# Performance work log

Measured on AMD Instinct MI355X. Metric: run time of the kernel, lower is better.

Reference implementation:

```python
import jax, jax.numpy as jnp
import numpy as np

N_NODES = 50000
IN_C = 128
OUT_C = 128
N_EDGES = 1600000
NEG_SLOPE = 0.2
EPS = 1e-16  # matches torch_geometric softmax denominator epsilon


def setup_inputs() -> dict:
    key = jax.random.key(0)
    k1, k2, k3, k4, k5 = jax.random.split(key, 5)
    glorot = 1.0 / np.sqrt(IN_C)
    x = jax.random.normal(k1, (N_NODES, IN_C), dtype=jnp.float32)
    W = jax.random.normal(k2, (IN_C, OUT_C), dtype=jnp.float32) * glorot
    a_src = jax.random.normal(k3, (OUT_C,), dtype=jnp.float32) * glorot
    a_dst = jax.random.normal(k4, (OUT_C,), dtype=jnp.float32) * glorot
    bias = jnp.zeros((OUT_C,), dtype=jnp.float32)
    edge_index = jax.random.randint(k5, (2, N_EDGES), 0, N_NODES, dtype=jnp.int32)
    return {"x": x, "W": W, "a_src": a_src, "a_dst": a_dst,
            "bias": bias, "edge_index": edge_index}


def reference(x, W, a_src, a_dst, bias, edge_index):
    N = x.shape[0]
    # add self loops (GATConv default add_self_loops=True)
    loops = jnp.arange(N, dtype=edge_index.dtype)
    src = jnp.concatenate([edge_index[0], loops])  # [E+N]
    dst = jnp.concatenate([edge_index[1], loops])

    h = x @ W                                      # [N, out]
    alpha_s = h @ a_src                            # [N]
    alpha_d = h @ a_dst                            # [N]

    e = alpha_s[src] + alpha_d[dst]                # [E+N]
    e = jnp.where(e > 0, e, NEG_SLOPE * e)         # leaky_relu

    # neighbor-wise (per destination node) stable softmax
    m = jax.ops.segment_max(e, dst, num_segments=N)
    ex = jnp.exp(e - m[dst])
    denom = jax.ops.segment_sum(ex, dst, num_segments=N)
    alpha = ex / (denom[dst] + EPS)

    # weighted aggregation of source features into destination nodes
    msgs = h[src] * alpha[:, None]                 # [E+N, out]
    out = jax.ops.segment_sum(msgs, dst, num_segments=N) + bias
    return jax.nn.relu(out)
```

## Files before the change

### kernel.cpp

```cpp
#include <hip/hip_runtime.h>
#include <hip/hip_fp16.h>

#define C 128
#define NEG_SLOPE 0.2f
#define SM_EPS 1e-16f
#define BKT_SHIFT 8
#define BKT_MASK 255
#define WP 136

typedef unsigned int uint32;
typedef __attribute__((ext_vector_type(8))) short bf16x8;
typedef __attribute__((ext_vector_type(4))) float f32x4;

static __device__ __forceinline__ unsigned short f2bf(float f) {
    uint32 u = __float_as_uint(f);
    uint32 r = 0x7FFFu + ((u >> 16) & 1u);
    return (unsigned short)((u + r) >> 16);
}
static __device__ __forceinline__ uint32 f2bf2(float lo, float hi) {
    return (uint32)f2bf(lo) | ((uint32)f2bf(hi) << 16);
}
static __device__ __forceinline__ uint32 f2h(float f) {
    __half h = __float2half(f);
    return (uint32)*reinterpret_cast<unsigned short*>(&h);
}
static __device__ __forceinline__ float h2f(uint32 b) {
    unsigned short s = (unsigned short)(b & 0xffffu);
    __half h = *reinterpret_cast<__half*>(&s);
    return __half2float(h);
}

__global__ __launch_bounds__(256) void cvtw_kernel(const float* __restrict__ W,
                                                   uint32* __restrict__ Wf) {
    int gid = blockIdx.x * 256 + threadIdx.x;
    int j2   = gid & 3;
    int lane = (gid >> 2) & 63;
    int tile = gid >> 8;
    int t = tile >> 2, kk = tile & 3;
    int n = t * 16 + (lane & 15);
    int k = kk * 32 + (lane >> 4) * 8 + j2 * 2;
    Wf[gid] = f2bf2(W[k * C + n], W[(k + 1) * C + n]);
}

__global__ __launch_bounds__(256) void gemm_hist_kernel(
    const float* __restrict__ x, const uint32* __restrict__ Wf,
    const float* __restrict__ a_src, const float* __restrict__ a_dst,
    unsigned short* __restrict__ hb, float* __restrict__ as_out,
    float* __restrict__ ad_out, int N,
    const int* __restrict__ dst, int* __restrict__ H,
    int E, int total, int chunkE)
{
    __shared__ __align__(16) unsigned short slice[4][16 * WP];
    __shared__ int lhist[256];

    const int tid  = threadIdx.x;
    const int lane = tid & 63;
    const int w    = tid >> 6;
    const int row0 = blockIdx.x * 64;
    const int m16  = lane & 15;
    const int q    = lane >> 4;

    lhist[tid] = 0;

    const int row = row0 + w * 16 + m16;
    const bool rv = (row < N);
    const float* xr_p = x + (size_t)(rv ? row : 0) * C + q * 8;

    float4 xr[8];
    #pragma unroll
    for (int kk = 0; kk < 4; ++kk) {
        xr[kk * 2]     = rv ? *(const float4*)(xr_p + kk * 32)     : make_float4(0, 0, 0, 0);
        xr[kk * 2 + 1] = rv ? *(const float4*)(xr_p + kk * 32 + 4) : make_float4(0, 0, 0, 0);
    }

    f32x4 acc[8];
    const f32x4 zz = {0.f, 0.f, 0.f, 0.f};
    #pragma unroll
    for (int t = 0; t < 8; ++t) acc[t] = zz;

    #pragma unroll
    for (int kk = 0; kk < 4; ++kk) {
        union { bf16x8 v; uint32 u[4]; } au;
        float4 p0 = xr[kk * 2], p1 = xr[kk * 2 + 1];
        au.u[0] = f2bf2(p0.x, p0.y); au.u[1] = f2bf2(p0.z, p0.w);
        au.u[2] = f2bf2(p1.x, p1.y); au.u[3] = f2bf2(p1.z, p1.w);
        #pragma unroll
        for (int t = 0; t < 8; ++t) {
            bf16x8 b = *(const bf16x8*)&Wf[((t * 4 + kk) * 64 + lane) * 4];
            acc[t] = __builtin_amdgcn_mfma_f32_16x16x32_bf16(au.v, b, acc[t], 0, 0, 0);
        }
    }

    float ps[4] = {0.f, 0.f, 0.f, 0.f}, pd[4] = {0.f, 0.f, 0.f, 0.f};
    #pragma unroll
    for (int t = 0; t < 8; ++t) {
        float av = a_src[t * 16 + m16];
        float dv = a_dst[t * 16 + m16];
        #pragma unroll
        for (int r = 0; r < 4; ++r) {
            ps[r] += acc[t][r] * av;
            pd[r] += acc[t][r] * dv;
        }
    }
    #pragma unroll
    for (int r = 0; r < 4; ++r) {
        #pragma unroll
        for (int off = 1; off < 16; off <<= 1) {
            ps[r] += __shfl_xor(ps[r], off, 64);
            pd[r] += __shfl_xor(pd[r], off, 64);
        }
    }
    if (m16 == 0) {
        #pragma unroll
        for (int r = 0; r < 4; ++r) {
            int rr = row0 + w * 16 + q * 4 + r;
            if (rr < N) { as_out[rr] = ps[r]; ad_out[rr] = pd[r]; }
        }
    }

    #pragma unroll
    for (int t = 0; t < 8; ++t)
        #pragma unroll
        for (int r = 0; r < 4; ++r)
            slice[w][(q * 4 + r) * WP + t * 16 + m16] = f2bf(acc[t][r]);
    __syncthreads();
    #pragma unroll
    for (int it = 0; it < 4; ++it) {
        int r = it * 4 + q;
        int rr = row0 + w * 16 + r;
        if (rr < N) {
            bf16x8 v = *(const bf16x8*)&slice[w][r * WP + m16 * 8];
            *(bf16x8*)&hb[(size_t)rr * C + m16 * 8] = v;
        }
    }

    const int c = blockIdx.x;
    const int start = c * chunkE;
    const int end = min(start + chunkE, total);
    for (int i = start + tid; i < end; i += 256) {
        int d = (i < E) ? dst[i] : (i - E);
        atomicAdd(&lhist[d >> BKT_SHIFT], 1);
    }
    __syncthreads();
    H[c * 256 + tid] = lhist[tid];
}

__global__ __launch_bounds__(1024) void scan_cols_kernel(
    int* __restrict__ H, int* __restrict__ colTot, int nchunk)
{
    __shared__ int wt[16];
    const int tid  = threadIdx.x;
    const int lane = tid & 63;
    const int w    = tid >> 6;
    const int col  = blockIdx.x;
    int v = (tid < nchunk) ? H[tid * 256 + col] : 0;
    int x = v;
    #pragma unroll
    for (int o = 1; o < 64; o <<= 1) {
        int t = __shfl_up(x, o, 64);
        if (lane >= o) x += t;
    }
    if (lane == 63) wt[w] = x;
    __syncthreads();
    int wbase = 0;
    #pragma unroll
    for (int w2 = 0; w2 < 16; ++w2) wbase += (w2 < w) ? wt[w2] : 0;
    int e = wbase + x - v;
    if (tid < nchunk) H[tid * 256 + col] = e;
    if (tid == nchunk - 1) colTot[col] = e + v;
}

__global__ __launch_bounds__(256) void scan_off_kernel(
    const int* __restrict__ colTot, int* __restrict__ bucket_off, int total)
{
    __shared__ int wt[4];
    const int tid = threadIdx.x;
    const int lane = tid & 63;
    const int w = tid >> 6;
    int v = colTot[tid];
    int x = v;
    #pragma unroll
    for (int o = 1; o < 64; o <<= 1) {
        int t = __shfl_up(x, o, 64);
        if (lane >= o) x += t;
    }
    if (lane == 63) wt[w] = x;
    __syncthreads();
    int wbase = 0;
    #pragma unroll
    for (int w2 = 0; w2 < 4; ++w2) wbase += (w2 < w) ? wt[w2] : 0;
    bucket_off[tid] = wbase + x - v;
    if (tid == 0) bucket_off[256] = total;
}

__global__ __launch_bounds__(256) void bin_kernel(
    const int* __restrict__ src, const int* __restrict__ dst,
    const int* __restrict__ bucket_off, const int* __restrict__ H,
    uint32* __restrict__ packed, int E, int total, int chunkE)
{
    __shared__ int lhist[256];
    __shared__ int base[256];
    const int tid = threadIdx.x;
    const int c = blockIdx.x;
    const int start = c * chunkE;
    const int end = min(start + chunkE, total);

    lhist[tid] = 0;
    __syncthreads();
    for (int i = start + tid; i < end; i += 256) {
        int d = (i < E) ? dst[i] : (i - E);
        atomicAdd(&lhist[d >> BKT_SHIFT], 1);
    }
    __syncthreads();
    base[tid] = bucket_off[tid] + H[c * 256 + tid];
    lhist[tid] = 0;
    __syncthreads();
    for (int i = start + tid; i < end; i += 256) {
        int s = (i < E) ? src[i] : (i - E);
        int d = (i < E) ? dst[i] : (i - E);
        int b = d >> BKT_SHIFT;
        int pos = base[b] + atomicAdd(&lhist[b], 1);
        packed[pos] = ((uint32)s << BKT_SHIFT) | (uint32)(d & BKT_MASK);
    }
}

__global__ __launch_bounds__(1024) void build_kernel(
    const uint32* __restrict__ packed, const int* __restrict__ bucket_off,
    const float* __restrict__ as, const float* __restrict__ ad,
    int* __restrict__ row_start, uint32* __restrict__ csr, int N, int NB, int total)
{
    __shared__ int cnt[256];
    __shared__ int cur[256];
    __shared__ float adl[256];
    __shared__ int wt[4];
    const int tid = threadIdx.x;
    const int b = blockIdx.x;

    if (tid < 256) {
        cnt[tid] = 0;
        int g = (b << BKT_SHIFT) + tid;
        adl[tid] = (g < N) ? ad[g] : 0.f;
    }
    __syncthreads();
    const int off = bucket_off[b];
    const int end = bucket_off[b + 1];
    if (b == 0 && tid == 0) row_start[N] = total;

    for (int j = off + tid; j < end; j += 1024)
        atomicAdd(&cnt[packed[j] & BKT_MASK], 1);
    __syncthreads();

    int v2 = 0, x2 = 0;
    if (tid < 256) {
        const int lane = tid & 63;
        v2 = cnt[tid]; x2 = v2;
        #pragma unroll
        for (int o = 1; o < 64; o <<= 1) {
            int t = __shfl_up(x2, o, 64);
            if (lane >= o) x2 += t;
        }
        if (lane == 63) wt[tid >> 6] = x2;
    }
    __syncthreads();
    if (tid < 256) {
        const int w = tid >> 6;
        int wbase = 0;
        #pragma unroll
        for (int w2 = 0; w2 < 4; ++w2) wbase += (w2 < w) ? wt[w2] : 0;
        int excl = wbase + x2 - v2;
        int g = (b << BKT_SHIFT) + tid;
        if (g < N) row_start[g] = off + excl;
        cur[tid] = excl;
    }
    __syncthreads();

    for (int j = off + tid; j < end; j += 1024) {
        uint32 p = packed[j];
        int l = (int)(p & BKT_MASK);
        int s = (int)(p >> BKT_SHIFT);
        float e = as[s] + adl[l];
        e = (e > 0.f) ? e : NEG_SLOPE * e;
        int pos = atomicAdd(&cur[l], 1);
        csr[off + pos] = ((uint32)s << 16) | f2h(e);
    }
}

static __device__ __forceinline__ void gather_node_fw(
    int d, const uint32* __restrict__ csr, const int* __restrict__ row_start,
    const unsigned short* __restrict__ hb, const float* __restrict__ bias,
    float* __restrict__ out, int lane)
{
    const int beg = row_start[d];
    const int deg = row_start[d + 1] - beg;
    const int c2 = lane << 1;
    float a0 = 0.f, a1 = 0.f;
    float m = -INFINITY;
    for (int t = lane; t < deg; t += 64) m = fmaxf(m, h2f(csr[beg + t]));
    #pragma unroll
    for (int off = 32; off > 0; off >>= 1) m = fmaxf(m, __shfl_xor(m, off, 64));
    float ssum = 0.f;
    for (int t = lane; t < deg; t += 64) ssum += __expf(h2f(csr[beg + t]) - m);
    #pragma unroll
    for (int off = 32; off > 0; off >>= 1) ssum += __shfl_xor(ssum, off, 64);
    float inv = 1.f / (ssum + SM_EPS);
    for (int t0 = 0; t0 < deg; t0 += 64) {
        int nc = min(64, deg - t0);
        uint32 ent = (lane < nc) ? csr[beg + t0 + lane] : 0xFC00u;
        float wl = (lane < nc) ? __expf(h2f(ent) - m) * inv : 0.f;
        uint32 bc = (ent & 0xffff0000u) | f2h(wl);
        for (int t = 0; t < nc; ++t) {
            uint32 b0 = (uint32)__shfl((int)bc, t, 64);
            uint32 u0 = *(const uint32*)&hb[(size_t)(b0 >> 16) * C + c2];
            float w0 = h2f(b0);
            a0 += __uint_as_float(u0 << 16) * w0;
            a1 += __uint_as_float(u0 & 0xffff0000u) * w0;
        }
    }
    float2 b2 = *(const float2*)&bias[c2];
    a0 = fmaxf(a0 + b2.x, 0.f);
    a1 = fmaxf(a1 + b2.y, 0.f);
    *(float2*)&out[(size_t)d * C + c2] = make_float2(a0, a1);
}

#define ACC4(r, wgt)                                           \
    {                                                          \
        a0 += __uint_as_float((r).x << 16)         * (wgt);    \
        a1 += __uint_as_float((r).x & 0xffff0000u) * (wgt);    \
        a2 += __uint_as_float((r).y << 16)         * (wgt);    \
        a3 += __uint_as_float((r).y & 0xffff0000u) * (wgt);    \
    }

__global__ __launch_bounds__(256) void gather_kernel(
    const uint32* __restrict__ csr, const int* __restrict__ row_start,
    const unsigned short* __restrict__ hb, const float* __restrict__ bias,
    float* __restrict__ out, int N)
{
    __shared__ __align__(16) uint2 lent[4][2][64];
    const int w    = threadIdx.x >> 6;
    const int lane = threadIdx.x & 63;
    const int half = lane >> 5;
    const int hl   = lane & 31;
    const int pair = blockIdx.x * 4 + w;
    const int d0 = pair * 2;
    if (d0 >= N) return;
    const int d = d0 + half;
    const bool valid = (d < N);

    int beg = 0, deg = 0;
    if (valid) { beg = row_start[d]; deg = row_start[d + 1] - beg; }

    int wdeg = deg;
    #pragma unroll
    for (int off = 32; off > 0; off >>= 1) wdeg = max(wdeg, __shfl_xor(wdeg, off, 64));

    if (wdeg > 64) {
        gather_node_fw(d0, csr, row_start, hb, bias, out, lane);
        if (d0 + 1 < N) gather_node_fw(d0 + 1, csr, row_start, hb, bias, out, lane);
        return;
    }

    uint32 ent0 = (hl < deg) ? csr[beg + hl] : 0xFC00u;
    uint32 ent1 = (32 + hl < deg) ? csr[beg + 32 + hl] : 0xFC00u;
    float e0 = h2f(ent0), e1 = h2f(ent1);
    float m = fmaxf(e0, e1);
    #pragma unroll
    for (int off = 16; off > 0; off >>= 1) m = fmaxf(m, __shfl_xor(m, off, 64));
    float p0 = (hl < deg) ? __expf(e0 - m) : 0.f;
    float p1 = (32 + hl < deg) ? __expf(e1 - m) : 0.f;
    float ssum = p0 + p1;
    #pragma unroll
    for (int off = 16; off > 0; off >>= 1) ssum += __shfl_xor(ssum, off, 64);
    const float inv = 1.f / (ssum + SM_EPS);

    lent[w][half][hl]      = make_uint2((ent0 & 0xffff0000u) >> 8, __float_as_uint(p0 * inv));
    lent[w][half][32 + hl] = make_uint2((ent1 & 0xffff0000u) >> 8, __float_as_uint(p1 * inv));
    __builtin_amdgcn_wave_barrier();

    const uint32 cb = (uint32)(hl << 3);
    const char* hbB = (const char*)hb;
    const uint2* lp = &lent[w][half][0];
    float a0 = 0.f, a1 = 0.f, a2 = 0.f, a3 = 0.f;

    int t = 0;
    for (; t + 8 <= deg; t += 8) {
        uint4 q0 = *(const uint4*)(lp + t);
        uint4 q1 = *(const uint4*)(lp + t + 2);
        uint4 q2 = *(const uint4*)(lp + t + 4);
        uint4 q3 = *(const uint4*)(lp + t + 6);
        uint2 r0 = *(const uint2*)(hbB + (q0.x + cb));
        uint2 r1 = *(const uint2*)(hbB + (q0.z + cb));
        uint2 r2 = *(const uint2*)(hbB + (q1.x + cb));
        uint2 r3 = *(const uint2*)(hbB + (q1.z + cb));
        uint2 r4 = *(const uint2*)(hbB + (q2.x + cb));
        uint2 r5 = *(const uint2*)(hbB + (q2.z + cb));
        uint2 r6 = *(const uint2*)(hbB + (q3.x + cb));
        uint2 r7 = *(const uint2*)(hbB + (q3.z + cb));
        float w0 = __uint_as_float(q0.y), w1 = __uint_as_float(q0.w);
        float w2 = __uint_as_float(q1.y), w3 = __uint_as_float(q1.w);
        float w4 = __uint_as_float(q2.y), w5 = __uint_as_float(q2.w);
        float w6 = __uint_as_float(q3.y), w7 = __uint_as_float(q3.w);
        ACC4(r0, w0) ACC4(r1, w1) ACC4(r2, w2) ACC4(r3, w3)
        ACC4(r4, w4) ACC4(r5, w5) ACC4(r6, w6) ACC4(r7, w7)
    }
    for (; t < deg; ++t) {
        uint2 q = lp[t];
        uint2 r = *(const uint2*)(hbB + (q.x + cb));
        float wt = __uint_as_float(q.y);
        ACC4(r, wt)
    }

    if (valid) {
        const int c4 = hl << 2;
        float4 bb = *(const float4*)&bias[c4];
        float4 o;
        o.x = fmaxf(a0 + bb.x, 0.f);
        o.y = fmaxf(a1 + bb.y, 0.f);
        o.z = fmaxf(a2 + bb.z, 0.f);
        o.w = fmaxf(a3 + bb.w, 0.f);
        *(float4*)&out[(size_t)d * C + c4] = o;
    }
}

extern "C" void kernel_launch(void* const* d_in, const int* in_sizes, int n_in,
                              void* d_out, int out_size, void* d_ws, size_t ws_size,
                              hipStream_t stream) {
    const float* x     = (const float*)d_in[0];
    const float* W     = (const float*)d_in[1];
    const float* a_src = (const float*)d_in[2];
    const float* a_dst = (const float*)d_in[3];
    const float* bias  = (const float*)d_in[4];
    const int*   edge  = (const int*)d_in[5];

    const int N = in_sizes[0] / C;
    const int E = in_sizes[5] / 2;
    const int total = E + N;
    const int* src = edge;
    const int* dst = edge + E;
    float* out = (float*)d_out;

    const int NB = (N + BKT_MASK) >> BKT_SHIFT;
    const int ntile = (N + 63) / 64;
    const int chunkE = (total + ntile - 1) / ntile;

    float* ws = (float*)d_ws;
    unsigned short* hb = (unsigned short*)ws;
    float* as = (float*)(hb + (size_t)N * C);
    float* ad = as + N;
    int* row_start = (int*)(ad + N);
    uint32* packed = (uint32*)(row_start + (N + 2));
    uint32* csr    = packed + total;
    uint32* Wf     = csr + total;
    int* colTot    = (int*)(Wf + 8192);
    int* bucket_off = colTot + 256;
    int* H          = bucket_off + 257;

    cvtw_kernel<<<32, 256, 0, stream>>>(W, Wf);
    gemm_hist_kernel<<<ntile, 256, 0, stream>>>(
        x, Wf, a_src, a_dst, hb, as, ad, N, dst, H, E, total, chunkE);
    scan_cols_kernel<<<256, 1024, 0, stream>>>(H, colTot, ntile);
    scan_off_kernel<<<1, 256, 0, stream>>>(colTot, bucket_off, total);
    bin_kernel<<<ntile, 256, 0, stream>>>(
        src, dst, bucket_off, H, packed, E, total, chunkE);
    build_kernel<<<NB, 1024, 0, stream>>>(packed, bucket_off, as, ad, row_start,
                                          csr, N, NB, total);
    gather_kernel<<<((N + 1) / 2 + 3) / 4, 256, 0, stream>>>(csr, row_start, hb, bias, out, N);
}
```

Before: 187.6 us.

## Fold bucket-offset scan into bin/build kernels, drop redundant histogram, widen gather to 4 nodes/wave

Removes the single-block scan_off kernel by having each bin_kernel and build_kernel block recompute the 256-entry bucket offset scan from colTot locally. bin_kernel also drops its first local-histogram pass, which was not needed because the per-chunk offsets already come from H. gather_kernel now handles four destination nodes per wave with 16 lanes each, and each lane loads 16-byte rows covering 8 channels. This aims to cut a kernel launch, one pass over dst, and per-edge load instructions. In exchange the scan work is duplicated in every block, and each node gets fewer lanes for its softmax.

```diff
diff --git a/kernel.cpp b/kernel.cpp
--- a/kernel.cpp
+++ b/kernel.cpp
@@ -170,13 +170,21 @@
     if (tid == nchunk - 1) colTot[col] = e + v;
 }
 
-__global__ __launch_bounds__(256) void scan_off_kernel(
-    const int* __restrict__ colTot, int* __restrict__ bucket_off, int total)
-{
+__global__ __launch_bounds__(256) void bin_kernel(
+    const int* __restrict__ src, const int* __restrict__ dst,
+    const int* __restrict__ colTot, const int* __restrict__ H,
+    uint32* __restrict__ packed, int E, int total, int chunkE)
+{
+    __shared__ int lhist[256];
+    __shared__ int base[256];
     __shared__ int wt[4];
     const int tid = threadIdx.x;
     const int lane = tid & 63;
     const int w = tid >> 6;
+    const int c = blockIdx.x;
+    const int start = c * chunkE;
+    const int end = min(start + chunkE, total);
+
     int v = colTot[tid];
     int x = v;
     #pragma unroll
@@ -185,36 +193,14 @@
         if (lane >= o) x += t;
     }
     if (lane == 63) wt[w] = x;
+    lhist[tid] = 0;
     __syncthreads();
     int wbase = 0;
     #pragma unroll
     for (int w2 = 0; w2 < 4; ++w2) wbase += (w2 < w) ? wt[w2] : 0;
-    bucket_off[tid] = wbase + x - v;
-    if (tid == 0) bucket_off[256] = total;
-}
-
-__global__ __launch_bounds__(256) void bin_kernel(
-    const int* __restrict__ src, const int* __restrict__ dst,
-    const int* __restrict__ bucket_off, const int* __restrict__ H,
-    uint32* __restrict__ packed, int E, int total, int chunkE)
-{
-    __shared__ int lhist[256];
-    __shared__ int base[256];
-    const int tid = threadIdx.x;
-    const int c = blockIdx.x;
-    const int start = c * chunkE;
-    const int end = min(start + chunkE, total);
-
-    lhist[tid] = 0;
-    __syncthreads();
-    for (int i = start + tid; i < end; i += 256) {
-        int d = (i < E) ? dst[i] : (i - E);
-        atomicAdd(&lhist[d >> BKT_SHIFT], 1);
-    }
-    __syncthreads();
-    base[tid] = bucket_off[tid] + H[c * 256 + tid];
-    lhist[tid] = 0;
-    __syncthreads();
+    base[tid] = (wbase + x - v) + H[c * 256 + tid];
+    __syncthreads();
+
     for (int i = start + tid; i < end; i += 256) {
         int s = (i < E) ? src[i] : (i - E);
         int d = (i < E) ? dst[i] : (i - E);
@@ -225,7 +211,7 @@
 }
 
 __global__ __launch_bounds__(1024) void build_kernel(
-    const uint32* __restrict__ packed, const int* __restrict__ bucket_off,
+    const uint32* __restrict__ packed, const int* __restrict__ colTot,
     const float* __restrict__ as, const float* __restrict__ ad,
     int* __restrict__ row_start, uint32* __restrict__ csr, int N, int NB, int total)
 {
@@ -233,17 +219,37 @@
     __shared__ int cur[256];
     __shared__ float adl[256];
     __shared__ int wt[4];
+    __shared__ int boff[257];
     const int tid = threadIdx.x;
     const int b = blockIdx.x;
 
+    int v0 = 0, x0 = 0;
     if (tid < 256) {
+        const int lane = tid & 63;
+        v0 = colTot[tid]; x0 = v0;
+        #pragma unroll
+        for (int o = 1; o < 64; o <<= 1) {
+            int t = __shfl_up(x0, o, 64);
+            if (lane >= o) x0 += t;
+        }
+        if (lane == 63) wt[tid >> 6] = x0;
         cnt[tid] = 0;
         int g = (b << BKT_SHIFT) + tid;
         adl[tid] = (g < N) ? ad[g] : 0.f;
     }
     __syncthreads();
-    const int off = bucket_off[b];
-    const int end = bucket_off[b + 1];
+    if (tid < 256) {
+        const int w = tid >> 6;
+        int wbase = 0;
+        #pragma unroll
+        for (int w2 = 0; w2 < 4; ++w2) wbase += (w2 < w) ? wt[w2] : 0;
+        boff[tid] = wbase + x0 - v0;
+        if (tid == 0) boff[256] = total;
+    }
+    __syncthreads();
+
+    const int off = boff[b];
+    const int end = boff[b + 1];
     if (b == 0 && tid == 0) row_start[N] = total;
 
     for (int j = off + tid; j < end; j += 1024)
@@ -322,12 +328,16 @@
     *(float2*)&out[(size_t)d * C + c2] = make_float2(a0, a1);
 }
 
-#define ACC4(r, wgt)                                           \
+#define ACC8(r, wgt)                                           \
     {                                                          \
         a0 += __uint_as_float((r).x << 16)         * (wgt);    \
         a1 += __uint_as_float((r).x & 0xffff0000u) * (wgt);    \
         a2 += __uint_as_float((r).y << 16)         * (wgt);    \
         a3 += __uint_as_float((r).y & 0xffff0000u) * (wgt);    \
+        a4 += __uint_as_float((r).z << 16)         * (wgt);    \
+        a5 += __uint_as_float((r).z & 0xffff0000u) * (wgt);    \
+        a6 += __uint_as_float((r).w << 16)         * (wgt);    \
+        a7 += __uint_as_float((r).w & 0xffff0000u) * (wgt);    \
     }
 
 __global__ __launch_bounds__(256) void gather_kernel(
@@ -335,15 +345,15 @@
     const unsigned short* __restrict__ hb, const float* __restrict__ bias,
     float* __restrict__ out, int N)
 {
-    __shared__ __align__(16) uint2 lent[4][2][64];
+    __shared__ __align__(16) uint2 lent[4][4][66];
     const int w    = threadIdx.x >> 6;
     const int lane = threadIdx.x & 63;
-    const int half = lane >> 5;
-    const int hl   = lane & 31;
-    const int pair = blockIdx.x * 4 + w;
-    const int d0 = pair * 2;
+    const int qt   = lane >> 4;
+    const int ql   = lane & 15;
+    const int quad = blockIdx.x * 4 + w;
+    const int d0 = quad * 4;
     if (d0 >= N) return;
-    const int d = d0 + half;
+    const int d = d0 + qt;
     const bool valid = (d < N);
 
     int beg = 0, deg = 0;
@@ -354,70 +364,84 @@
     for (int off = 32; off > 0; off >>= 1) wdeg = max(wdeg, __shfl_xor(wdeg, off, 64));
 
     if (wdeg > 64) {
-        gather_node_fw(d0, csr, row_start, hb, bias, out, lane);
-        if (d0 + 1 < N) gather_node_fw(d0 + 1, csr, row_start, hb, bias, out, lane);
+        #pragma unroll
+        for (int k = 0; k < 4; ++k)
+            if (d0 + k < N) gather_node_fw(d0 + k, csr, row_start, hb, bias, out, lane);
         return;
     }
 
-    uint32 ent0 = (hl < deg) ? csr[beg + hl] : 0xFC00u;
-    uint32 ent1 = (32 + hl < deg) ? csr[beg + 32 + hl] : 0xFC00u;
-    float e0 = h2f(ent0), e1 = h2f(ent1);
-    float m = fmaxf(e0, e1);
-    #pragma unroll
-    for (int off = 16; off > 0; off >>= 1) m = fmaxf(m, __shfl_xor(m, off, 64));
-    float p0 = (hl < deg) ? __expf(e0 - m) : 0.f;
-    float p1 = (32 + hl < deg) ? __expf(e1 - m) : 0.f;
-    float ssum = p0 + p1;
-    #pragma unroll
-    for (int off = 16; off > 0; off >>= 1) ssum += __shfl_xor(ssum, off, 64);
+    uint32 ent0 = (ql < deg) ? csr[beg + ql] : 0xFC00u;
+    uint32 ent1 = (16 + ql < deg) ? csr[beg + 16 + ql] : 0xFC00u;
+    uint32 ent2 = (32 + ql < deg) ? csr[beg + 32 + ql] : 0xFC00u;
+    uint32 ent3 = (48 + ql < deg) ? csr[beg + 48 + ql] : 0xFC00u;
+    float e0 = h2f(ent0), e1 = h2f(ent1), e2 = h2f(ent2), e3 = h2f(ent3);
+    float m = fmaxf(fmaxf(e0, e1), fmaxf(e2, e3));
+    #pragma unroll
+    for (int off = 8; off > 0; off >>= 1) m = fmaxf(m, __shfl_xor(m, off, 64));
+    float p0 = (ql < deg) ? __expf(e0 - m) : 0.f;
+    float p1 = (16 + ql < deg) ? __expf(e1 - m) : 0.f;
+    float p2 = (32 + ql < deg) ? __expf(e2 - m) : 0.f;
+    float p3 = (48 + ql < deg) ? __expf(e3 - m) : 0.f;
+    float ssum = (p0 + p1) + (p2 + p3);
+    #pragma unroll
+    for (int off = 8; off > 0; off >>= 1) ssum += __shfl_xor(ssum, off, 64);
     const float inv = 1.f / (ssum + SM_EPS);
 
-    lent[w][half][hl]      = make_uint2((ent0 & 0xffff0000u) >> 8, __float_as_uint(p0 * inv));
-    lent[w][half][32 + hl] = make_uint2((ent1 & 0xffff0000u) >> 8, __float_as_uint(p1 * inv));
+    uint2* lq = &lent[w][qt][0];
+    lq[ql]      = make_uint2((ent0 & 0xffff0000u) >> 8, __float_as_uint(p0 * inv));
+    lq[16 + ql] = make_uint2((ent1 & 0xffff0000u) >> 8, __float_as_uint(p1 * inv));
+    lq[32 + ql] = make_uint2((ent2 & 0xffff0000u) >> 8, __float_as_uint(p2 * inv));
+    lq[48 + ql] = make_uint2((ent3 & 0xffff0000u) >> 8, __float_as_uint(p3 * inv));
     __builtin_amdgcn_wave_barrier();
 
-    const uint32 cb = (uint32)(hl << 3);
+    const uint32 cb = (uint32)(ql << 4);
     const char* hbB = (const char*)hb;
-    const uint2* lp = &lent[w][half][0];
     float a0 = 0.f, a1 = 0.f, a2 = 0.f, a3 = 0.f;
+    float a4 = 0.f, a5 = 0.f, a6 = 0.f, a7 = 0.f;
 
     int t = 0;
     for (; t + 8 <= deg; t += 8) {
-        uint4 q0 = *(const uint4*)(lp + t);
-        uint4 q1 = *(const uint4*)(lp + t + 2);
-        uint4 q2 = *(const uint4*)(lp + t + 4);
-        uint4 q3 = *(const uint4*)(lp + t + 6);
-        uint2 r0 = *(const uint2*)(hbB + (q0.x + cb));
-        uint2 r1 = *(const uint2*)(hbB + (q0.z + cb));
-        uint2 r2 = *(const uint2*)(hbB + (q1.x + cb));
-        uint2 r3 = *(const uint2*)(hbB + (q1.z + cb));
-        uint2 r4 = *(const uint2*)(hbB + (q2.x + cb));
-        uint2 r5 = *(const uint2*)(hbB + (q2.z + cb));
-        uint2 r6 = *(const uint2*)(hbB + (q3.x + cb));
-        uint2 r7 = *(const uint2*)(hbB + (q3.z + cb));
+        uint4 q0 = *(const uint4*)(lq + t);
+        uint4 q1 = *(const uint4*)(lq + t + 2);
+        uint4 q2 = *(const uint4*)(lq + t + 4);
+        uint4 q3 = *(const uint4*)(lq + t + 6);
+        uint4 r0 = *(const uint4*)(hbB + (q0.x + cb));
+        uint4 r1 = *(const uint4*)(hbB + (q0.z + cb));
+        uint4 r2 = *(const uint4*)(hbB + (q1.x + cb));
+        uint4 r3 = *(const uint4*)(hbB + (q1.z + cb));
+        uint4 r4 = *(const uint4*)(hbB + (q2.x + cb));
+        uint4 r5 = *(const uint4*)(hbB + (q2.z + cb));
+        uint4 r6 = *(const uint4*)(hbB + (q3.x + cb));
+        uint4 r7 = *(const uint4*)(hbB + (q3.z + cb));
         float w0 = __uint_as_float(q0.y), w1 = __uint_as_float(q0.w);
         float w2 = __uint_as_float(q1.y), w3 = __uint_as_float(q1.w);
         float w4 = __uint_as_float(q2.y), w5 = __uint_as_float(q2.w);
         float w6 = __uint_as_float(q3.y), w7 = __uint_as_float(q3.w);
-        ACC4(r0, w0) ACC4(r1, w1) ACC4(r2, w2) ACC4(r3, w3)
-        ACC4(r4, w4) ACC4(r5, w5) ACC4(r6, w6) ACC4(r7, w7)
+        ACC8(r0, w0) ACC8(r1, w1) ACC8(r2, w2) ACC8(r3, w3)
+        ACC8(r4, w4) ACC8(r5, w5) ACC8(r6, w6) ACC8(r7, w7)
     }
     for (; t < deg; ++t) {
-        uint2 q = lp[t];
-        uint2 r = *(const uint2*)(hbB + (q.x + cb));
-        float wt = __uint_as_float(q.y);
-        ACC4(r, wt)
+        uint2 qv = lq[t];
+        uint4 r = *(const uint4*)(hbB + (qv.x + cb));
+        float wt2 = __uint_as_float(qv.y);
+        ACC8(r, wt2)
     }
 
     if (valid) {
-        const int c4 = hl << 2;
-        float4 bb = *(const float4*)&bias[c4];
-        float4 o;
-        o.x = fmaxf(a0 + bb.x, 0.f);
-        o.y = fmaxf(a1 + bb.y, 0.f);
-        o.z = fmaxf(a2 + bb.z, 0.f);
-        o.w = fmaxf(a3 + bb.w, 0.f);
-        *(float4*)&out[(size_t)d * C + c4] = o;
+        const int c8 = ql << 3;
+        float4 b0 = *(const float4*)&bias[c8];
+        float4 b1 = *(const float4*)&bias[c8 + 4];
+        float4 o0, o1;
+        o0.x = fmaxf(a0 + b0.x, 0.f);
+        o0.y = fmaxf(a1 + b0.y, 0.f);
+        o0.z = fmaxf(a2 + b0.z, 0.f);
+        o0.w = fmaxf(a3 + b0.w, 0.f);
+        o1.x = fmaxf(a4 + b1.x, 0.f);
+        o1.y = fmaxf(a5 + b1.y, 0.f);
+        o1.z = fmaxf(a6 + b1.z, 0.f);
+        o1.w = fmaxf(a7 + b1.w, 0.f);
+        *(float4*)&out[(size_t)d * C + c8] = o0;
+        *(float4*)&out[(size_t)d * C + c8 + 4] = o1;
     }
 }
 
@@ -451,17 +475,15 @@
     uint32* csr    = packed + total;
     uint32* Wf     = csr + total;
     int* colTot    = (int*)(Wf + 8192);
-    int* bucket_off = colTot + 256;
-    int* H          = bucket_off + 257;
+    int* H         = colTot + 256;
 
     cvtw_kernel<<<32, 256, 0, stream>>>(W, Wf);
     gemm_hist_kernel<<<ntile, 256, 0, stream>>>(
         x, Wf, a_src, a_dst, hb, as, ad, N, dst, H, E, total, chunkE);
     scan_cols_kernel<<<256, 1024, 0, stream>>>(H, colTot, ntile);
-    scan_off_kernel<<<1, 256, 0, stream>>>(colTot, bucket_off, total);
     bin_kernel<<<ntile, 256, 0, stream>>>(
-        src, dst, bucket_off, H, packed, E, total, chunkE);
-    build_kernel<<<NB, 1024, 0, stream>>>(packed, bucket_off, as, ad, row_start,
+        src, dst, colTot, H, packed, E, total, chunkE);
+    build_kernel<<<NB, 1024, 0, stream>>>(packed, colTot, as, ad, row_start,
                                           csr, N, NB, total);
-    gather_kernel<<<((N + 1) / 2 + 3) / 4, 256, 0, stream>>>(csr, row_start, hb, bias, out, N);
-}
+    gather_kernel<<<((N + 3) / 4 + 3) / 4, 256, 0, stream>>>(csr, row_start, hb, bias, out, N);
+}
```

New measurement: 186.9 us. About the same (-0.4%).

## Fuse GEMM with edge binning and fold offset scan into consumers

Applied to the files above, without the earlier changes.

The weight conversion is merged into the histogram kernel, and the feature GEMM is merged with the edge-binning pass. Blocks of the merged kernel are specialized by block index, so the dense GEMM runs alongside the scatter-heavy binning. The separate single-block offset scan kernel is removed: bin blocks and build blocks each recompute the 256-entry prefix scan of bucket totals locally. The redundant per-chunk histogram recount in the binning pass is also dropped. This cuts the launch count and the serialization between stages, at the cost of duplicated small scans in every block.

```diff
diff --git a/kernel.cpp b/kernel.cpp
--- a/kernel.cpp
+++ b/kernel.cpp
@@ -30,111 +30,27 @@
     return __half2float(h);
 }
 
-__global__ __launch_bounds__(256) void cvtw_kernel(const float* __restrict__ W,
-                                                   uint32* __restrict__ Wf) {
-    int gid = blockIdx.x * 256 + threadIdx.x;
-    int j2   = gid & 3;
-    int lane = (gid >> 2) & 63;
-    int tile = gid >> 8;
-    int t = tile >> 2, kk = tile & 3;
-    int n = t * 16 + (lane & 15);
-    int k = kk * 32 + (lane >> 4) * 8 + j2 * 2;
-    Wf[gid] = f2bf2(W[k * C + n], W[(k + 1) * C + n]);
-}
-
-__global__ __launch_bounds__(256) void gemm_hist_kernel(
-    const float* __restrict__ x, const uint32* __restrict__ Wf,
-    const float* __restrict__ a_src, const float* __restrict__ a_dst,
-    unsigned short* __restrict__ hb, float* __restrict__ as_out,
-    float* __restrict__ ad_out, int N,
+__global__ __launch_bounds__(256) void cvtw_hist_kernel(
+    const float* __restrict__ W, uint32* __restrict__ Wf,
     const int* __restrict__ dst, int* __restrict__ H,
-    int E, int total, int chunkE)
-{
-    __shared__ __align__(16) unsigned short slice[4][16 * WP];
+    int E, int total, int nchunk, int chunkE)
+{
     __shared__ int lhist[256];
-
-    const int tid  = threadIdx.x;
-    const int lane = tid & 63;
-    const int w    = tid >> 6;
-    const int row0 = blockIdx.x * 64;
-    const int m16  = lane & 15;
-    const int q    = lane >> 4;
-
+    const int tid = threadIdx.x;
     lhist[tid] = 0;
-
-    const int row = row0 + w * 16 + m16;
-    const bool rv = (row < N);
-    const float* xr_p = x + (size_t)(rv ? row : 0) * C + q * 8;
-
-    float4 xr[8];
-    #pragma unroll
-    for (int kk = 0; kk < 4; ++kk) {
-        xr[kk * 2]     = rv ? *(const float4*)(xr_p + kk * 32)     : make_float4(0, 0, 0, 0);
-        xr[kk * 2 + 1] = rv ? *(const float4*)(xr_p + kk * 32 + 4) : make_float4(0, 0, 0, 0);
-    }
-
-    f32x4 acc[8];
-    const f32x4 zz = {0.f, 0.f, 0.f, 0.f};
-    #pragma unroll
-    for (int t = 0; t < 8; ++t) acc[t] = zz;
-
-    #pragma unroll
-    for (int kk = 0; kk < 4; ++kk) {
-        union { bf16x8 v; uint32 u[4]; } au;
-        float4 p0 = xr[kk * 2], p1 = xr[kk * 2 + 1];
-        au.u[0] = f2bf2(p0.x, p0.y); au.u[1] = f2bf2(p0.z, p0.w);
-        au.u[2] = f2bf2(p1.x, p1.y); au.u[3] = f2bf2(p1.z, p1.w);
-        #pragma unroll
-        for (int t = 0; t < 8; ++t) {
-            bf16x8 b = *(const bf16x8*)&Wf[((t * 4 + kk) * 64 + lane) * 4];
-            acc[t] = __builtin_amdgcn_mfma_f32_16x16x32_bf16(au.v, b, acc[t], 0, 0, 0);
-        }
-    }
-
-    float ps[4] = {0.f, 0.f, 0.f, 0.f}, pd[4] = {0.f, 0.f, 0.f, 0.f};
-    #pragma unroll
-    for (int t = 0; t < 8; ++t) {
-        float av = a_src[t * 16 + m16];
-        float dv = a_dst[t * 16 + m16];
-        #pragma unroll
-        for (int r = 0; r < 4; ++r) {
-            ps[r] += acc[t][r] * av;
-            pd[r] += acc[t][r] * dv;
-        }
-    }
-    #pragma unroll
-    for (int r = 0; r < 4; ++r) {
-        #pragma unroll
-        for (int off = 1; off < 16; off <<= 1) {
-            ps[r] += __shfl_xor(ps[r], off, 64);
-            pd[r] += __shfl_xor(pd[r], off, 64);
-        }
-    }
-    if (m16 == 0) {
-        #pragma unroll
-        for (int r = 0; r < 4; ++r) {
-            int rr = row0 + w * 16 + q * 4 + r;
-            if (rr < N) { as_out[rr] = ps[r]; ad_out[rr] = pd[r]; }
-        }
-    }
-
-    #pragma unroll
-    for (int t = 0; t < 8; ++t)
-        #pragma unroll
-        for (int r = 0; r < 4; ++r)
-            slice[w][(q * 4 + r) * WP + t * 16 + m16] = f2bf(acc[t][r]);
-    __syncthreads();
-    #pragma unroll
-    for (int it = 0; it < 4; ++it) {
-        int r = it * 4 + q;
-        int rr = row0 + w * 16 + r;
-        if (rr < N) {
-            bf16x8 v = *(const bf16x8*)&slice[w][r * WP + m16 * 8];
-            *(bf16x8*)&hb[(size_t)rr * C + m16 * 8] = v;
-        }
-    }
-
+    const int gid = blockIdx.x * 256 + tid;
+    if (gid < 8192) {
+        int j2   = gid & 3;
+        int lane = (gid >> 2) & 63;
+        int tile = gid >> 8;
+        int t = tile >> 2, kk = tile & 3;
+        int n = t * 16 + (lane & 15);
+        int k = kk * 32 + (lane >> 4) * 8 + j2 * 2;
+        Wf[gid] = f2bf2(W[k * C + n], W[(k + 1) * C + n]);
+    }
     const int c = blockIdx.x;
+    if (c >= nchunk) return;
+    __syncthreads();
     const int start = c * chunkE;
     const int end = min(start + chunkE, total);
     for (int i = start + tid; i < end; i += 256) {
@@ -170,62 +86,133 @@
     if (tid == nchunk - 1) colTot[col] = e + v;
 }
 
-__global__ __launch_bounds__(256) void scan_off_kernel(
-    const int* __restrict__ colTot, int* __restrict__ bucket_off, int total)
-{
-    __shared__ int wt[4];
-    const int tid = threadIdx.x;
-    const int lane = tid & 63;
-    const int w = tid >> 6;
-    int v = colTot[tid];
-    int x = v;
-    #pragma unroll
-    for (int o = 1; o < 64; o <<= 1) {
-        int t = __shfl_up(x, o, 64);
-        if (lane >= o) x += t;
-    }
-    if (lane == 63) wt[w] = x;
-    __syncthreads();
-    int wbase = 0;
-    #pragma unroll
-    for (int w2 = 0; w2 < 4; ++w2) wbase += (w2 < w) ? wt[w2] : 0;
-    bucket_off[tid] = wbase + x - v;
-    if (tid == 0) bucket_off[256] = total;
-}
-
-__global__ __launch_bounds__(256) void bin_kernel(
+__global__ __launch_bounds__(256) void gemm_bin_kernel(
+    const float* __restrict__ x, const uint32* __restrict__ Wf,
+    const float* __restrict__ a_src, const float* __restrict__ a_dst,
+    unsigned short* __restrict__ hb, float* __restrict__ as_out,
+    float* __restrict__ ad_out, int N,
     const int* __restrict__ src, const int* __restrict__ dst,
-    const int* __restrict__ bucket_off, const int* __restrict__ H,
-    uint32* __restrict__ packed, int E, int total, int chunkE)
-{
+    const int* __restrict__ colTot, const int* __restrict__ H,
+    uint32* __restrict__ packed, int E, int total, int ntile, int chunkE)
+{
+    __shared__ __align__(16) unsigned short slice[4][16 * WP];
     __shared__ int lhist[256];
     __shared__ int base[256];
-    const int tid = threadIdx.x;
-    const int c = blockIdx.x;
-    const int start = c * chunkE;
-    const int end = min(start + chunkE, total);
-
-    lhist[tid] = 0;
-    __syncthreads();
-    for (int i = start + tid; i < end; i += 256) {
-        int d = (i < E) ? dst[i] : (i - E);
-        atomicAdd(&lhist[d >> BKT_SHIFT], 1);
-    }
-    __syncthreads();
-    base[tid] = bucket_off[tid] + H[c * 256 + tid];
-    lhist[tid] = 0;
-    __syncthreads();
-    for (int i = start + tid; i < end; i += 256) {
-        int s = (i < E) ? src[i] : (i - E);
-        int d = (i < E) ? dst[i] : (i - E);
-        int b = d >> BKT_SHIFT;
-        int pos = base[b] + atomicAdd(&lhist[b], 1);
-        packed[pos] = ((uint32)s << BKT_SHIFT) | (uint32)(d & BKT_MASK);
+    __shared__ int wt[4];
+
+    const int tid  = threadIdx.x;
+    const int lane = tid & 63;
+    const int w    = tid >> 6;
+
+    if (blockIdx.x < (unsigned)ntile) {
+        const int row0 = blockIdx.x * 64;
+        const int m16  = lane & 15;
+        const int q    = lane >> 4;
+
+        const int row = row0 + w * 16 + m16;
+        const bool rv = (row < N);
+        const float* xr_p = x + (size_t)(rv ? row : 0) * C + q * 8;
+
+        float4 xr[8];
+        #pragma unroll
+        for (int kk = 0; kk < 4; ++kk) {
+            xr[kk * 2]     = rv ? *(const float4*)(xr_p + kk * 32)     : make_float4(0, 0, 0, 0);
+            xr[kk * 2 + 1] = rv ? *(const float4*)(xr_p + kk * 32 + 4) : make_float4(0, 0, 0, 0);
+        }
+
+        f32x4 acc[8];
+        const f32x4 zz = {0.f, 0.f, 0.f, 0.f};
+        #pragma unroll
+        for (int t = 0; t < 8; ++t) acc[t] = zz;
+
+        #pragma unroll
+        for (int kk = 0; kk < 4; ++kk) {
+            union { bf16x8 v; uint32 u[4]; } au;
+            float4 p0 = xr[kk * 2], p1 = xr[kk * 2 + 1];
+            au.u[0] = f2bf2(p0.x, p0.y); au.u[1] = f2bf2(p0.z, p0.w);
+            au.u[2] = f2bf2(p1.x, p1.y); au.u[3] = f2bf2(p1.z, p1.w);
+            #pragma unroll
+            for (int t = 0; t < 8; ++t) {
+                bf16x8 b = *(const bf16x8*)&Wf[((t * 4 + kk) * 64 + lane) * 4];
+                acc[t] = __builtin_amdgcn_mfma_f32_16x16x32_bf16(au.v, b, acc[t], 0, 0, 0);
+            }
+        }
+
+        float ps[4] = {0.f, 0.f, 0.f, 0.f}, pd[4] = {0.f, 0.f, 0.f, 0.f};
+        #pragma unroll
+        for (int t = 0; t < 8; ++t) {
+            float av = a_src[t * 16 + m16];
+            float dv = a_dst[t * 16 + m16];
+            #pragma unroll
+            for (int r = 0; r < 4; ++r) {
+                ps[r] += acc[t][r] * av;
+                pd[r] += acc[t][r] * dv;
+            }
+        }
+        #pragma unroll
+        for (int r = 0; r < 4; ++r) {
+            #pragma unroll
+            for (int off = 1; off < 16; off <<= 1) {
+                ps[r] += __shfl_xor(ps[r], off, 64);
+                pd[r] += __shfl_xor(pd[r], off, 64);
+            }
+        }
+        if (m16 == 0) {
+            #pragma unroll
+            for (int r = 0; r < 4; ++r) {
+                int rr = row0 + w * 16 + q * 4 + r;
+                if (rr < N) { as_out[rr] = ps[r]; ad_out[rr] = pd[r]; }
+            }
+        }
+
+        #pragma unroll
+        for (int t = 0; t < 8; ++t)
+            #pragma unroll
+            for (int r = 0; r < 4; ++r)
+                slice[w][(q * 4 + r) * WP + t * 16 + m16] = f2bf(acc[t][r]);
+        __syncthreads();
+        #pragma unroll
+        for (int it = 0; it < 4; ++it) {
+            int r = it * 4 + q;
+            int rr = row0 + w * 16 + r;
+            if (rr < N) {
+                bf16x8 v = *(const bf16x8*)&slice[w][r * WP + m16 * 8];
+                *(bf16x8*)&hb[(size_t)rr * C + m16 * 8] = v;
+            }
+        }
+    } else {
+        const int c = blockIdx.x - ntile;
+        const int start = c * chunkE;
+        const int end = min(start + chunkE, total);
+
+        int v = colTot[tid];
+        int xx = v;
+        #pragma unroll
+        for (int o = 1; o < 64; o <<= 1) {
+            int t = __shfl_up(xx, o, 64);
+            if (lane >= o) xx += t;
+        }
+        if (lane == 63) wt[w] = xx;
+        lhist[tid] = 0;
+        __syncthreads();
+        int wbase = 0;
+        #pragma unroll
+        for (int w2 = 0; w2 < 4; ++w2) wbase += (w2 < w) ? wt[w2] : 0;
+        base[tid] = (wbase + xx - v) + H[c * 256 + tid];
+        __syncthreads();
+
+        for (int i = start + tid; i < end; i += 256) {
+            int s = (i < E) ? src[i] : (i - E);
+            int d = (i < E) ? dst[i] : (i - E);
+            int b = d >> BKT_SHIFT;
+            int pos = base[b] + atomicAdd(&lhist[b], 1);
+            packed[pos] = ((uint32)s << BKT_SHIFT) | (uint32)(d & BKT_MASK);
+        }
     }
 }
 
 __global__ __launch_bounds__(1024) void build_kernel(
-    const uint32* __restrict__ packed, const int* __restrict__ bucket_off,
+    const uint32* __restrict__ packed, const int* __restrict__ colTot,
     const float* __restrict__ as, const float* __restrict__ ad,
     int* __restrict__ row_start, uint32* __restrict__ csr, int N, int NB, int total)
 {
@@ -233,17 +220,37 @@
     __shared__ int cur[256];
     __shared__ float adl[256];
     __shared__ int wt[4];
+    __shared__ int boff[257];
     const int tid = threadIdx.x;
     const int b = blockIdx.x;
 
+    int v0 = 0, x0 = 0;
     if (tid < 256) {
+        const int lane = tid & 63;
+        v0 = colTot[tid]; x0 = v0;
+        #pragma unroll
+        for (int o = 1; o < 64; o <<= 1) {
+            int t = __shfl_up(x0, o, 64);
+            if (lane >= o) x0 += t;
+        }
+        if (lane == 63) wt[tid >> 6] = x0;
         cnt[tid] = 0;
         int g = (b << BKT_SHIFT) + tid;
         adl[tid] = (g < N) ? ad[g] : 0.f;
     }
     __syncthreads();
-    const int off = bucket_off[b];
-    const int end = bucket_off[b + 1];
+    if (tid < 256) {
+        const int w = tid >> 6;
+        int wbase = 0;
+        #pragma unroll
+        for (int w2 = 0; w2 < 4; ++w2) wbase += (w2 < w) ? wt[w2] : 0;
+        boff[tid] = wbase + x0 - v0;
+        if (tid == 0) boff[256] = total;
+    }
+    __syncthreads();
+
+    const int off = boff[b];
+    const int end = boff[b + 1];
     if (b == 0 && tid == 0) row_start[N] = total;
 
     for (int j = off + tid; j < end; j += 1024)
@@ -451,17 +458,16 @@
     uint32* csr    = packed + total;
     uint32* Wf     = csr + total;
     int* colTot    = (int*)(Wf + 8192);
-    int* bucket_off = colTot + 256;
-    int* H          = bucket_off + 257;
-
-    cvtw_kernel<<<32, 256, 0, stream>>>(W, Wf);
-    gemm_hist_kernel<<<ntile, 256, 0, stream>>>(
-        x, Wf, a_src, a_dst, hb, as, ad, N, dst, H, E, total, chunkE);
+    int* H         = colTot + 256;
+
+    const int grid1 = (ntile > 32) ? ntile : 32;
+
+    cvtw_hist_kernel<<<grid1, 256, 0, stream>>>(W, Wf, dst, H, E, total, ntile, chunkE);
     scan_cols_kernel<<<256, 1024, 0, stream>>>(H, colTot, ntile);
-    scan_off_kernel<<<1, 256, 0, stream>>>(colTot, bucket_off, total);
-    bin_kernel<<<ntile, 256, 0, stream>>>(
-        src, dst, bucket_off, H, packed, E, total, chunkE);
-    build_kernel<<<NB, 1024, 0, stream>>>(packed, bucket_off, as, ad, row_start,
+    gemm_bin_kernel<<<2 * ntile, 256, 0, stream>>>(
+        x, Wf, a_src, a_dst, hb, as, ad, N, src, dst,
+        colTot, H, packed, E, total, ntile, chunkE);
+    build_kernel<<<NB, 1024, 0, stream>>>(packed, colTot, as, ad, row_start,
                                           csr, N, NB, total);
     gather_kernel<<<((N + 1) / 2 + 3) / 4, 256, 0, stream>>>(csr, row_start, hb, bias, out, N);
 }
```

Measured after the change: 182.2 us, median of 2. -2.9%, faster.
